# Optimization experiments

Hardware: AMD Instinct MI355X
Metric: run time of the kernel (lower is better)

## Reference

```python
import jax, jax.numpy as jnp
import numpy as np

N_NODES = 50000
N_EDGES = 800000
IN_CH = 128
HIDDEN = 16
HEADS = 8
OUT_CH = 128
EDGE_DIM = 16


def _lin_params(key, fan_in, fan_out, bias=True):
    k1, k2 = jax.random.split(key)
    s = 1.0 / np.sqrt(fan_in)
    W = jax.random.uniform(k1, (fan_in, fan_out), jnp.float32, -s, s)
    if bias:
        b = jax.random.uniform(k2, (fan_out,), jnp.float32, -s, s)
        return W, b
    return W


def setup_inputs() -> dict:
    key = jax.random.key(0)
    ks = jax.random.split(key, 16)
    x = jax.random.normal(ks[0], (N_NODES, IN_CH), jnp.float32)
    edge_index = jax.random.randint(ks[1], (2, N_EDGES), 0, N_NODES, jnp.int64)
    edge_attr = jax.random.normal(ks[2], (N_EDGES, EDGE_DIM), jnp.float32)
    HC0 = HEADS * HIDDEN
    Wq0, bq0 = _lin_params(ks[3], IN_CH, HC0)
    Wk0, bk0 = _lin_params(ks[4], IN_CH, HC0)
    Wv0, bv0 = _lin_params(ks[5], IN_CH, HC0)
    We0 = _lin_params(ks[6], EDGE_DIM, HC0, bias=False)
    Ws0, bs0 = _lin_params(ks[7], IN_CH, HC0)
    Wq1, bq1 = _lin_params(ks[8], HC0, OUT_CH)
    Wk1, bk1 = _lin_params(ks[9], HC0, OUT_CH)
    Wv1, bv1 = _lin_params(ks[10], HC0, OUT_CH)
    We1 = _lin_params(ks[11], EDGE_DIM, OUT_CH, bias=False)
    Ws1, bs1 = _lin_params(ks[12], HC0, OUT_CH)
    return dict(x=x, edge_index=edge_index, edge_attr=edge_attr,
                Wq0=Wq0, bq0=bq0, Wk0=Wk0, bk0=bk0, Wv0=Wv0, bv0=bv0, We0=We0, Ws0=Ws0, bs0=bs0,
                Wq1=Wq1, bq1=bq1, Wk1=Wk1, bk1=bk1, Wv1=Wv1, bv1=bv1, We1=We1, Ws1=Ws1, bs1=bs1)


def transformer_conv(x, src, dst, edge_attr, Wq, bq, Wk, bk, Wv, bv, We, Ws, bs, heads, concat):
    """PyG TransformerConv: gather-attend-softmax(per dst)-scatter, edge features added to key/value."""
    N = x.shape[0]
    E = src.shape[0]
    C = Wq.shape[1] // heads
    q = (x @ Wq + bq).reshape(N, heads, C)
    k = (x @ Wk + bk).reshape(N, heads, C)
    v = (x @ Wv + bv).reshape(N, heads, C)
    e = (edge_attr @ We).reshape(E, heads, C)
    key_e = k[src] + e                                  # [E,H,C]
    alpha = jnp.sum(q[dst] * key_e, axis=-1) / jnp.sqrt(jnp.asarray(C, x.dtype))  # [E,H]
    # segment softmax over incoming edges of each dst node
    m = jax.ops.segment_max(alpha, dst, num_segments=N)       # [N,H]
    p = jnp.exp(alpha - m[dst])
    denom = jax.ops.segment_sum(p, dst, num_segments=N)       # [N,H]
    w = p / (denom[dst] + 1e-16)                              # [E,H]
    msg = (v[src] + e) * w[..., None]                         # [E,H,C]
    agg = jax.ops.segment_sum(msg.reshape(E, heads * C), dst, num_segments=N).reshape(N, heads, C)
    out = agg.reshape(N, heads * C) if concat else agg.mean(axis=1)
    return out + (x @ Ws + bs)                                # root skip connection


def reference(x, edge_index, edge_attr,
              Wq0, bq0, Wk0, bk0, Wv0, bv0, We0, Ws0, bs0,
              Wq1, bq1, Wk1, bk1, Wv1, bv1, We1, Ws1, bs1):
    src, dst = edge_index[0], edge_index[1]
    h = transformer_conv(x, src, dst, edge_attr, Wq0, bq0, Wk0, bk0, Wv0, bv0, We0, Ws0, bs0,
                         heads=HEADS, concat=True)
    h = jax.nn.relu(h)
    out = transformer_conv(h, src, dst, edge_attr, Wq1, bq1, Wk1, bk1, Wv1, bv1, We1, Ws1, bs1,
                           heads=1, concat=False)
    return out
```

## Files before the change

### kernel.cpp

```cpp
#include <hip/hip_runtime.h>
#include <stdint.h>

#define N_NODES 50000
#define N_EDGES 800000

typedef __bf16 bf16x8 __attribute__((ext_vector_type(8)));
typedef float f32x4 __attribute__((ext_vector_type(4)));

__device__ __forceinline__ unsigned short f2bf(float f) {
  union { float f; unsigned int i; } x; x.f = f;
  unsigned int i = x.i;
  unsigned int r = (i + 0x7fffu + ((i >> 16) & 1u)) >> 16;
  return (unsigned short)r;
}
__device__ __forceinline__ float bfl(unsigned int p) {
  union { unsigned int i; float f; } x; x.i = p << 16; return x.f;
}
__device__ __forceinline__ float bfh(unsigned int p) {
  union { unsigned int i; float f; } x; x.i = p & 0xffff0000u; return x.f;
}

struct Ptr8 { const float* p[8]; };

__global__ __launch_bounds__(256) void transpose_w(Ptr8 ws, unsigned short* wt) {
  int mat = blockIdx.x;
  const float* W = ws.p[mat];
  unsigned short* out = wt + mat * 16384;
  for (int it = 0; it < 64; ++it) {
    int idx = it * 256 + threadIdx.x;
    int n = idx >> 7, k = idx & 127;
    out[n * 128 + k] = f2bf(W[k * 128 + n]);
  }
}

__global__ void zero_kernel(int* cnt, int* cursor, int* pad) {
  int i = blockIdx.x * blockDim.x + threadIdx.x;
  if (i < N_NODES) { cnt[i] = 0; cursor[i] = 0; }
  if (i < 16) pad[i] = 0;
}

__global__ void hist_kernel(const int* __restrict__ dst, int* __restrict__ cnt) {
  int e = blockIdx.x * blockDim.x + threadIdx.x;
  if (e < N_EDGES) atomicAdd(&cnt[dst[e]], 1);
}

__global__ __launch_bounds__(1024) void scan_kernel(const int* __restrict__ cnt, int* __restrict__ rs) {
  const int n = N_NODES, per = 49;
  int t = threadIdx.x;
  int lo = t * per; int hi = lo + per;
  if (lo > n) lo = n;
  if (hi > n) hi = n;
  int s = 0;
  for (int i = lo; i < hi; ++i) s += cnt[i];
  int lane = t & 63, wv = t >> 6;
  int v = s;
  #pragma unroll
  for (int off = 1; off < 64; off <<= 1) {
    int u = __shfl_up(v, off, 64);
    if (lane >= off) v += u;
  }
  __shared__ int wsum[16], woff[16];
  if (lane == 63) wsum[wv] = v;
  __syncthreads();
  if (t == 0) { int a = 0; for (int w = 0; w < 16; ++w) { woff[w] = a; a += wsum[w]; } }
  __syncthreads();
  int run = woff[wv] + (v - s);
  if (t == 0) rs[0] = 0;
  for (int i = lo; i < hi; ++i) { run += cnt[i]; rs[i + 1] = run; }
}

__global__ void scatter_kernel(const int* __restrict__ src, const int* __restrict__ dst,
                               const int* __restrict__ rs, int* __restrict__ cursor,
                               int2* __restrict__ eidx2) {
  int e = blockIdx.x * blockDim.x + threadIdx.x;
  if (e < N_EDGES) {
    int d = dst[e];
    int pos = rs[d] + atomicAdd(&cursor[d], 1);
    eidx2[pos] = make_int2(src[e], e);
  }
}

struct GemmArgs {
  const float* Xf;
  const unsigned short* Xh;
  const unsigned short* Wt;
  const float* b0; const float* b1; const float* b2; const float* b3;
  unsigned short* qb;
  unsigned short* kvb;
  unsigned short* sb;
  int M;
};

template<bool XF32>
__global__ __launch_bounds__(256) void node_gemm(GemmArgs ga) {
  __shared__ alignas(16) unsigned short At[128 * 128];
  __shared__ alignas(16) unsigned short Bt[128 * 128];
  int which = blockIdx.y;
  const unsigned short* Wt = ga.Wt + which * 16384;
  int m0 = blockIdx.x * 128;

  #pragma unroll
  for (int it = 0; it < 8; ++it) {
    int c = it * 256 + threadIdx.x;
    int row = c >> 4, slot = c & 15;
    int dsl = slot ^ (row & 7);
    int grow = m0 + row; if (grow >= ga.M) grow = ga.M - 1;
    alignas(16) unsigned short tmp[8];
    if (XF32) {
      const float* xp = ga.Xf + (size_t)grow * 128 + slot * 8;
      float4 a = *(const float4*)xp;
      float4 b = *(const float4*)(xp + 4);
      tmp[0] = f2bf(a.x); tmp[1] = f2bf(a.y); tmp[2] = f2bf(a.z); tmp[3] = f2bf(a.w);
      tmp[4] = f2bf(b.x); tmp[5] = f2bf(b.y); tmp[6] = f2bf(b.z); tmp[7] = f2bf(b.w);
    } else {
      *(uint4*)tmp = *(const uint4*)(ga.Xh + (size_t)grow * 128 + slot * 8);
    }
    *(uint4*)(&At[row * 128 + dsl * 8]) = *(const uint4*)tmp;
    *(uint4*)(&Bt[row * 128 + dsl * 8]) = *(const uint4*)(Wt + c * 8);
  }
  __syncthreads();

  int lane = threadIdx.x & 63, wv = threadIdx.x >> 6;
  int wm = wv >> 1, wn = wv & 1;
  int lr = lane & 15, lk = lane >> 4;
  f32x4 acc[4][4];
  #pragma unroll
  for (int mi = 0; mi < 4; ++mi)
    #pragma unroll
    for (int ni = 0; ni < 4; ++ni) acc[mi][ni] = (f32x4){0.f, 0.f, 0.f, 0.f};

  #pragma unroll
  for (int kk = 0; kk < 4; ++kk) {
    bf16x8 af[4], bfr[4];
    #pragma unroll
    for (int mi = 0; mi < 4; ++mi) {
      int row = wm * 64 + mi * 16 + lr;
      int slot = (kk * 4 + lk) ^ (row & 7);
      af[mi] = *(const bf16x8*)(&At[row * 128 + slot * 8]);
    }
    #pragma unroll
    for (int ni = 0; ni < 4; ++ni) {
      int row = wn * 64 + ni * 16 + lr;
      int slot = (kk * 4 + lk) ^ (row & 7);
      bfr[ni] = *(const bf16x8*)(&Bt[row * 128 + slot * 8]);
    }
    #pragma unroll
    for (int mi = 0; mi < 4; ++mi)
      #pragma unroll
      for (int ni = 0; ni < 4; ++ni)
        acc[mi][ni] = __builtin_amdgcn_mfma_f32_16x16x32_bf16(af[mi], bfr[ni], acc[mi][ni], 0, 0, 0);
  }

  const float* bias = which == 0 ? ga.b0 : which == 1 ? ga.b1 : which == 2 ? ga.b2 : ga.b3;
  float bv[4];
  #pragma unroll
  for (int ni = 0; ni < 4; ++ni) bv[ni] = bias[wn * 64 + ni * 16 + lr];
  #pragma unroll
  for (int mi = 0; mi < 4; ++mi) {
    #pragma unroll
    for (int i = 0; i < 4; ++i) {
      int row = m0 + wm * 64 + mi * 16 + lk * 4 + i;
      if (row < ga.M) {
        #pragma unroll
        for (int ni = 0; ni < 4; ++ni) {
          int col = wn * 64 + ni * 16 + lr;
          unsigned short val = f2bf(acc[mi][ni][i] + bv[ni]);
          if (which == 0)      ga.qb[(size_t)row * 128 + col] = val;
          else if (which == 3) ga.sb[(size_t)row * 128 + col] = val;
          else {
            size_t base = (size_t)row * 256 + (size_t)(col >> 1) * 4 + (col & 1);
            ga.kvb[base + (which == 2 ? 2 : 0)] = val;
          }
        }
      }
    }
  }
}

template<int CHALF, bool RELU, bool OUT_BF16>
__global__ __launch_bounds__(256) void edge_attn(
    const unsigned short* __restrict__ Q, const uint2* __restrict__ KV,
    const unsigned short* __restrict__ S, const float* __restrict__ We,
    const float* __restrict__ EA, const int2* __restrict__ eidx2,
    const int* __restrict__ rs, void* __restrict__ outv, float inv_sqrt_c) {
  int wv = threadIdx.x >> 6, lane = threadIdx.x & 63;
  int node = blockIdx.x * 4 + wv;
  if (node >= N_NODES) return;
  int c0 = lane * 2;
  int jbase = (lane & 1) * 8 + ((lane >> 1) & 1) * 4 + ((lane >> 2) & 1) * 2;

  unsigned int qp = *(const unsigned int*)(Q + (size_t)node * 128 + c0);
  float qa = bfl(qp) * inv_sqrt_c;
  float qb = bfh(qp) * inv_sqrt_c;

  float part[16];
  #pragma unroll
  for (int j = 0; j < 16; ++j) {
    float2 wp = *(const float2*)(We + j * 128 + c0);
    part[j] = qa * wp.x + qb * wp.y;
  }
  {
    bool hi = lane & 1;
    #pragma unroll
    for (int j = 0; j < 8; ++j) {
      float kept = hi ? part[j + 8] : part[j];
      float sent = hi ? part[j] : part[j + 8];
      part[j] = kept + __shfl_xor(sent, 1, 64);
    }
    hi = lane & 2;
    #pragma unroll
    for (int j = 0; j < 4; ++j) {
      float kept = hi ? part[j + 4] : part[j];
      float sent = hi ? part[j] : part[j + 4];
      part[j] = kept + __shfl_xor(sent, 2, 64);
    }
    hi = lane & 4;
    #pragma unroll
    for (int j = 0; j < 2; ++j) {
      float kept = hi ? part[j + 2] : part[j];
      float sent = hi ? part[j] : part[j + 2];
      part[j] = kept + __shfl_xor(sent, 4, 64);
    }
  }
  if (CHALF == 64) {
    #pragma unroll
    for (int s = 8; s <= 32; s <<= 1) {
      part[0] += __shfl_xor(part[0], s, 64);
      part[1] += __shfl_xor(part[1], s, 64);
    }
  }
  float qw0 = part[0] * (CHALF == 64 ? 0.125f : 1.0f);
  float qw1 = part[1] * (CHALF == 64 ? 0.125f : 1.0f);

  int i0 = rs[node], i1 = rs[node + 1];
  int deg = i1 - i0;
  float den = 0.f, a0 = 0.f, a1 = 0.f, wea0 = 0.f, wea1 = 0.f;

  struct Buf { uint2 kv[8]; float ea0[8]; float ea1[8]; };
  Buf bA, bB;
  int2 ceA, ceB;

  auto load_ce = [&](int c) -> int2 {
    return eidx2[i0 + c * 8 + (lane & 7)];
  };
  auto gather = [&](Buf& b, const int2& ce) {
    #pragma unroll
    for (int j = 0; j < 8; ++j) {
      int sv = __shfl(ce.x, j, 64);
      int ei = __shfl(ce.y, j, 64);
      b.kv[j] = KV[(size_t)sv * 64 + lane];
      float2 ep = *(const float2*)(EA + (size_t)ei * 16 + jbase);
      b.ea0[j] = ep.x; b.ea1[j] = ep.y;
    }
  };
  auto compute = [&](const Buf& b, int c) {
    #pragma unroll
    for (int j = 0; j < 8; ++j) {
      int g = i0 + c * 8 + j;
      uint2 kv = b.kv[j];
      float p = qa * bfl(kv.x) + qb * bfh(kv.x) + qw0 * b.ea0[j] + qw1 * b.ea1[j];
      #pragma unroll
      for (int off = 1; off < CHALF; off <<= 1) p += __shfl_xor(p, off, 64);
      float w = (g < i1) ? __expf(p) : 0.f;
      den  += w;
      a0   += w * bfl(kv.y);
      a1   += w * bfh(kv.y);
      wea0 += w * b.ea0[j];
      wea1 += w * b.ea1[j];
    }
  };

  int nch = (deg + 7) >> 3;
  if (nch > 0) {
    ceA = load_ce(0);
    if (nch > 1) ceB = load_ce(1);
    gather(bA, ceA);
    int c = 0;
    while (true) {
      if (c + 1 < nch) gather(bB, ceB);
      if (c + 2 < nch) ceA = load_ce(c + 2);
      compute(bA, c);
      ++c; if (c >= nch) break;
      if (c + 1 < nch) gather(bA, ceA);
      if (c + 2 < nch) ceB = load_ce(c + 2);
      compute(bB, c);
      ++c; if (c >= nch) break;
    }
  }

  float inv = 1.f / (den + 1e-16f);
  float eadd0 = 0.f, eadd1 = 0.f;
  #pragma unroll
  for (int j = 0; j < 16; ++j) {
    int owner = ((j >> 3) & 1) | (((j >> 2) & 1) << 1) | (((j >> 1) & 1) << 2);
    int srcl = (lane & 56) | owner;
    float val = __shfl((j & 1) ? wea1 : wea0, srcl, 64);
    float2 wp = *(const float2*)(We + j * 128 + c0);
    eadd0 += val * wp.x;
    eadd1 += val * wp.y;
  }
  unsigned int sp = *(const unsigned int*)(S + (size_t)node * 128 + c0);
  float o0 = (a0 + eadd0) * inv + bfl(sp);
  float o1 = (a1 + eadd1) * inv + bfh(sp);
  if (RELU) { o0 = fmaxf(o0, 0.f); o1 = fmaxf(o1, 0.f); }
  if (OUT_BF16) {
    unsigned int op = ((unsigned int)f2bf(o1) << 16) | (unsigned int)f2bf(o0);
    *(unsigned int*)((unsigned short*)outv + (size_t)node * 128 + c0) = op;
  } else {
    *(float2*)((float*)outv + (size_t)node * 128 + c0) = make_float2(o0, o1);
  }
}

extern "C" void kernel_launch(void* const* d_in, const int* in_sizes, int n_in,
                              void* d_out, int out_size, void* d_ws, size_t ws_size,
                              hipStream_t stream) {
  const float* x   = (const float*)d_in[0];
  const int*   ei  = (const int*)d_in[1];
  const float* ea  = (const float*)d_in[2];
  const float* Wq0 = (const float*)d_in[3];
  const float* bq0 = (const float*)d_in[4];
  const float* Wk0 = (const float*)d_in[5];
  const float* bk0 = (const float*)d_in[6];
  const float* Wv0 = (const float*)d_in[7];
  const float* bv0 = (const float*)d_in[8];
  const float* We0 = (const float*)d_in[9];
  const float* Ws0 = (const float*)d_in[10];
  const float* bs0 = (const float*)d_in[11];
  const float* Wq1 = (const float*)d_in[12];
  const float* bq1 = (const float*)d_in[13];
  const float* Wk1 = (const float*)d_in[14];
  const float* bk1 = (const float*)d_in[15];
  const float* Wv1 = (const float*)d_in[16];
  const float* bv1 = (const float*)d_in[17];
  const float* We1 = (const float*)d_in[18];
  const float* Ws1 = (const float*)d_in[19];
  const float* bs1 = (const float*)d_in[20];

  char* ws = (char*)d_ws;
  size_t off = 0;
  auto alloc = [&](size_t bytes) -> void* {
    void* p = ws + off;
    off = (off + bytes + 255) & ~(size_t)255;
    return p;
  };
  unsigned short* WT  = (unsigned short*)alloc(8 * 16384 * 2);
  unsigned short* q   = (unsigned short*)alloc((size_t)N_NODES * 128 * 2);
  unsigned short* kvb = (unsigned short*)alloc((size_t)N_NODES * 256 * 2);
  unsigned short* s   = (unsigned short*)alloc((size_t)N_NODES * 128 * 2);
  unsigned short* h   = (unsigned short*)alloc((size_t)N_NODES * 128 * 2);
  int* cnt    = (int*)alloc(N_NODES * 4);
  int* rs     = (int*)alloc((N_NODES + 1) * 4);
  int* cursor = (int*)alloc(N_NODES * 4);
  int2* eidx2 = (int2*)alloc(((size_t)N_EDGES + 8) * 8);

  const int* srcp = ei;
  const int* dstp = ei + N_EDGES;

  Ptr8 p8 = {{Wq0, Wk0, Wv0, Ws0, Wq1, Wk1, Wv1, Ws1}};
  transpose_w<<<8, 256, 0, stream>>>(p8, WT);
  zero_kernel<<<196, 256, 0, stream>>>(cnt, cursor, (int*)(eidx2 + N_EDGES));
  hist_kernel<<<3125, 256, 0, stream>>>(dstp, cnt);
  scan_kernel<<<1, 1024, 0, stream>>>(cnt, rs);
  scatter_kernel<<<3125, 256, 0, stream>>>(srcp, dstp, rs, cursor, eidx2);

  GemmArgs ga0 = { x, nullptr, WT, bq0, bk0, bv0, bs0, q, kvb, s, N_NODES };
  node_gemm<true><<<dim3(391, 4), 256, 0, stream>>>(ga0);
  edge_attn<8, true, true><<<12500, 256, 0, stream>>>(q, (const uint2*)kvb, s, We0,
                                                      ea, eidx2, rs, h, 0.25f);

  GemmArgs ga1 = { nullptr, h, WT + 4 * 16384, bq1, bk1, bv1, bs1, q, kvb, s, N_NODES };
  node_gemm<false><<<dim3(391, 4), 256, 0, stream>>>(ga1);
  edge_attn<64, false, false><<<12500, 256, 0, stream>>>(q, (const uint2*)kvb, s, We1,
                                                         ea, eidx2, rs, d_out, 0.08838834764831845f);
}
```

Baseline: 672.8 us.

## Pre-gather edge attributes into CSR order as bf16 and fuse four node GEMMs

Adds an ea_gather pass that reorders edge_attr into dst-sorted CSR order as bf16. The attention kernels can then read edge features contiguously, without indexing 64-byte fp32 rows through an edge-id indirection. The node GEMM now loads the X tile once and loops over the four weight matrices, instead of launching four grid slices that each reload X. The interleaved KV buffer is split into separate K and V arrays. The cost is an extra pass over edges, about 25.6 MB of extra workspace, and a 4x smaller GEMM grid (391 blocks) that may lower occupancy and parallelism.

```diff
diff --git a/kernel.cpp b/kernel.cpp
--- a/kernel.cpp
+++ b/kernel.cpp
@@ -33,10 +33,11 @@
   }
 }
 
-__global__ void zero_kernel(int* cnt, int* cursor, int* pad) {
+__global__ void zero_kernel(int* cnt, int* cursor, int* srcpad, unsigned int* eapad) {
   int i = blockIdx.x * blockDim.x + threadIdx.x;
   if (i < N_NODES) { cnt[i] = 0; cursor[i] = 0; }
-  if (i < 16) pad[i] = 0;
+  if (i < 8)  srcpad[i] = 0;
+  if (i < 64) eapad[i] = 0;
 }
 
 __global__ void hist_kernel(const int* __restrict__ dst, int* __restrict__ cnt) {
@@ -71,33 +72,45 @@
 
 __global__ void scatter_kernel(const int* __restrict__ src, const int* __restrict__ dst,
                                const int* __restrict__ rs, int* __restrict__ cursor,
-                               int2* __restrict__ eidx2) {
+                               int* __restrict__ srcArr, int* __restrict__ eidxArr) {
   int e = blockIdx.x * blockDim.x + threadIdx.x;
   if (e < N_EDGES) {
     int d = dst[e];
     int pos = rs[d] + atomicAdd(&cursor[d], 1);
-    eidx2[pos] = make_int2(src[e], e);
-  }
-}
-
-struct GemmArgs {
+    srcArr[pos]  = src[e];
+    eidxArr[pos] = e;
+  }
+}
+
+__global__ __launch_bounds__(256) void ea_gather(const float* __restrict__ EA,
+                                                 const int* __restrict__ eidxArr,
+                                                 unsigned short* __restrict__ eacsr) {
+  int r = blockIdx.x * 32 + (threadIdx.x >> 3);
+  if (r >= N_EDGES) return;
+  int j = (threadIdx.x & 7) * 2;
+  int e = eidxArr[r];
+  float2 v = *(const float2*)(EA + (size_t)e * 16 + j);
+  unsigned int pk = (unsigned int)f2bf(v.x) | ((unsigned int)f2bf(v.y) << 16);
+  *(unsigned int*)(eacsr + (size_t)r * 16 + j) = pk;
+}
+
+struct Gemm4Args {
   const float* Xf;
   const unsigned short* Xh;
   const unsigned short* Wt;
-  const float* b0; const float* b1; const float* b2; const float* b3;
-  unsigned short* qb;
-  unsigned short* kvb;
-  unsigned short* sb;
+  const float* b[4];
+  unsigned short* o[4];
   int M;
 };
 
 template<bool XF32>
-__global__ __launch_bounds__(256) void node_gemm(GemmArgs ga) {
+__global__ __launch_bounds__(256) void node_gemm4(Gemm4Args ga) {
   __shared__ alignas(16) unsigned short At[128 * 128];
   __shared__ alignas(16) unsigned short Bt[128 * 128];
-  int which = blockIdx.y;
-  const unsigned short* Wt = ga.Wt + which * 16384;
   int m0 = blockIdx.x * 128;
+  int lane = threadIdx.x & 63, wv = threadIdx.x >> 6;
+  int wm = wv >> 1, wn = wv & 1;
+  int lr = lane & 15, lk = lane >> 4;
 
   #pragma unroll
   for (int it = 0; it < 8; ++it) {
@@ -116,60 +129,64 @@
       *(uint4*)tmp = *(const uint4*)(ga.Xh + (size_t)grow * 128 + slot * 8);
     }
     *(uint4*)(&At[row * 128 + dsl * 8]) = *(const uint4*)tmp;
-    *(uint4*)(&Bt[row * 128 + dsl * 8]) = *(const uint4*)(Wt + c * 8);
-  }
-  __syncthreads();
-
-  int lane = threadIdx.x & 63, wv = threadIdx.x >> 6;
-  int wm = wv >> 1, wn = wv & 1;
-  int lr = lane & 15, lk = lane >> 4;
-  f32x4 acc[4][4];
-  #pragma unroll
-  for (int mi = 0; mi < 4; ++mi)
-    #pragma unroll
-    for (int ni = 0; ni < 4; ++ni) acc[mi][ni] = (f32x4){0.f, 0.f, 0.f, 0.f};
-
-  #pragma unroll
-  for (int kk = 0; kk < 4; ++kk) {
-    bf16x8 af[4], bfr[4];
+  }
+
+  #pragma unroll
+  for (int which = 0; which < 4; ++which) {
+    if (which) __syncthreads();
+    const unsigned short* Wt = ga.Wt + which * 16384;
+    #pragma unroll
+    for (int it = 0; it < 8; ++it) {
+      int c = it * 256 + threadIdx.x;
+      int row = c >> 4, slot = c & 15;
+      int dsl = slot ^ (row & 7);
+      *(uint4*)(&Bt[row * 128 + dsl * 8]) = *(const uint4*)(Wt + c * 8);
+    }
+    __syncthreads();
+
+    f32x4 acc[4][4];
+    #pragma unroll
+    for (int mi = 0; mi < 4; ++mi)
+      #pragma unroll
+      for (int ni = 0; ni < 4; ++ni) acc[mi][ni] = (f32x4){0.f, 0.f, 0.f, 0.f};
+
+    #pragma unroll
+    for (int kk = 0; kk < 4; ++kk) {
+      bf16x8 af[4], bfr[4];
+      #pragma unroll
+      for (int mi = 0; mi < 4; ++mi) {
+        int row = wm * 64 + mi * 16 + lr;
+        int slot = (kk * 4 + lk) ^ (row & 7);
+        af[mi] = *(const bf16x8*)(&At[row * 128 + slot * 8]);
+      }
+      #pragma unroll
+      for (int ni = 0; ni < 4; ++ni) {
+        int row = wn * 64 + ni * 16 + lr;
+        int slot = (kk * 4 + lk) ^ (row & 7);
+        bfr[ni] = *(const bf16x8*)(&Bt[row * 128 + slot * 8]);
+      }
+      #pragma unroll
+      for (int mi = 0; mi < 4; ++mi)
+        #pragma unroll
+        for (int ni = 0; ni < 4; ++ni)
+          acc[mi][ni] = __builtin_amdgcn_mfma_f32_16x16x32_bf16(af[mi], bfr[ni], acc[mi][ni], 0, 0, 0);
+    }
+
+    const float* bias = ga.b[which];
+    unsigned short* outp = ga.o[which];
+    float bv[4];
+    #pragma unroll
+    for (int ni = 0; ni < 4; ++ni) bv[ni] = bias[wn * 64 + ni * 16 + lr];
     #pragma unroll
     for (int mi = 0; mi < 4; ++mi) {
-      int row = wm * 64 + mi * 16 + lr;
-      int slot = (kk * 4 + lk) ^ (row & 7);
-      af[mi] = *(const bf16x8*)(&At[row * 128 + slot * 8]);
-    }
-    #pragma unroll
-    for (int ni = 0; ni < 4; ++ni) {
-      int row = wn * 64 + ni * 16 + lr;
-      int slot = (kk * 4 + lk) ^ (row & 7);
-      bfr[ni] = *(const bf16x8*)(&Bt[row * 128 + slot * 8]);
-    }
-    #pragma unroll
-    for (int mi = 0; mi < 4; ++mi)
-      #pragma unroll
-      for (int ni = 0; ni < 4; ++ni)
-        acc[mi][ni] = __builtin_amdgcn_mfma_f32_16x16x32_bf16(af[mi], bfr[ni], acc[mi][ni], 0, 0, 0);
-  }
-
-  const float* bias = which == 0 ? ga.b0 : which == 1 ? ga.b1 : which == 2 ? ga.b2 : ga.b3;
-  float bv[4];
-  #pragma unroll
-  for (int ni = 0; ni < 4; ++ni) bv[ni] = bias[wn * 64 + ni * 16 + lr];
-  #pragma unroll
-  for (int mi = 0; mi < 4; ++mi) {
-    #pragma unroll
-    for (int i = 0; i < 4; ++i) {
-      int row = m0 + wm * 64 + mi * 16 + lk * 4 + i;
-      if (row < ga.M) {
-        #pragma unroll
-        for (int ni = 0; ni < 4; ++ni) {
-          int col = wn * 64 + ni * 16 + lr;
-          unsigned short val = f2bf(acc[mi][ni][i] + bv[ni]);
-          if (which == 0)      ga.qb[(size_t)row * 128 + col] = val;
-          else if (which == 3) ga.sb[(size_t)row * 128 + col] = val;
-          else {
-            size_t base = (size_t)row * 256 + (size_t)(col >> 1) * 4 + (col & 1);
-            ga.kvb[base + (which == 2 ? 2 : 0)] = val;
+      #pragma unroll
+      for (int i = 0; i < 4; ++i) {
+        int row = m0 + wm * 64 + mi * 16 + lk * 4 + i;
+        if (row < ga.M) {
+          #pragma unroll
+          for (int ni = 0; ni < 4; ++ni) {
+            int col = wn * 64 + ni * 16 + lr;
+            outp[(size_t)row * 128 + col] = f2bf(acc[mi][ni][i] + bv[ni]);
           }
         }
       }
@@ -179,10 +196,11 @@
 
 template<int CHALF, bool RELU, bool OUT_BF16>
 __global__ __launch_bounds__(256) void edge_attn(
-    const unsigned short* __restrict__ Q, const uint2* __restrict__ KV,
-    const unsigned short* __restrict__ S, const float* __restrict__ We,
-    const float* __restrict__ EA, const int2* __restrict__ eidx2,
-    const int* __restrict__ rs, void* __restrict__ outv, float inv_sqrt_c) {
+    const unsigned short* __restrict__ Q, const unsigned short* __restrict__ Kb,
+    const unsigned short* __restrict__ Vb, const unsigned short* __restrict__ S,
+    const float* __restrict__ We, const unsigned short* __restrict__ EAC,
+    const int* __restrict__ srcArr, const int* __restrict__ rs,
+    void* __restrict__ outv, float inv_sqrt_c) {
   int wv = threadIdx.x >> 6, lane = threadIdx.x & 63;
   int node = blockIdx.x * 4 + wv;
   if (node >= N_NODES) return;
@@ -190,6 +208,7 @@
   int jbase = (lane & 1) * 8 + ((lane >> 1) & 1) * 4 + ((lane >> 2) & 1) * 2;
 
   unsigned int qp = *(const unsigned int*)(Q + (size_t)node * 128 + c0);
+  unsigned int sp = *(const unsigned int*)(S + (size_t)node * 128 + c0);
   float qa = bfl(qp) * inv_sqrt_c;
   float qb = bfh(qp) * inv_sqrt_c;
 
@@ -236,53 +255,52 @@
   int deg = i1 - i0;
   float den = 0.f, a0 = 0.f, a1 = 0.f, wea0 = 0.f, wea1 = 0.f;
 
-  struct Buf { uint2 kv[8]; float ea0[8]; float ea1[8]; };
+  struct Buf { unsigned int kp[8], vp[8], ep[8]; };
   Buf bA, bB;
-  int2 ceA, ceB;
-
-  auto load_ce = [&](int c) -> int2 {
-    return eidx2[i0 + c * 8 + (lane & 7)];
+  int svA = 0, svB = 0;
+
+  auto load_src = [&](int c) -> int {
+    return srcArr[i0 + c * 8 + (lane & 7)];
   };
-  auto gather = [&](Buf& b, const int2& ce) {
+  auto gather = [&](Buf& b, int c, int sv) {
     #pragma unroll
     for (int j = 0; j < 8; ++j) {
-      int sv = __shfl(ce.x, j, 64);
-      int ei = __shfl(ce.y, j, 64);
-      b.kv[j] = KV[(size_t)sv * 64 + lane];
-      float2 ep = *(const float2*)(EA + (size_t)ei * 16 + jbase);
-      b.ea0[j] = ep.x; b.ea1[j] = ep.y;
+      int s = __shfl(sv, j, 8);
+      b.kp[j] = *(const unsigned int*)(Kb + (size_t)s * 128 + c0);
+      b.vp[j] = *(const unsigned int*)(Vb + (size_t)s * 128 + c0);
+      b.ep[j] = *(const unsigned int*)(EAC + (size_t)(i0 + c * 8 + j) * 16 + jbase);
     }
   };
   auto compute = [&](const Buf& b, int c) {
     #pragma unroll
     for (int j = 0; j < 8; ++j) {
       int g = i0 + c * 8 + j;
-      uint2 kv = b.kv[j];
-      float p = qa * bfl(kv.x) + qb * bfh(kv.x) + qw0 * b.ea0[j] + qw1 * b.ea1[j];
+      float ea0 = bfl(b.ep[j]), ea1 = bfh(b.ep[j]);
+      float p = qa * bfl(b.kp[j]) + qb * bfh(b.kp[j]) + qw0 * ea0 + qw1 * ea1;
       #pragma unroll
       for (int off = 1; off < CHALF; off <<= 1) p += __shfl_xor(p, off, 64);
       float w = (g < i1) ? __expf(p) : 0.f;
       den  += w;
-      a0   += w * bfl(kv.y);
-      a1   += w * bfh(kv.y);
-      wea0 += w * b.ea0[j];
-      wea1 += w * b.ea1[j];
+      a0   += w * bfl(b.vp[j]);
+      a1   += w * bfh(b.vp[j]);
+      wea0 += w * ea0;
+      wea1 += w * ea1;
     }
   };
 
   int nch = (deg + 7) >> 3;
   if (nch > 0) {
-    ceA = load_ce(0);
-    if (nch > 1) ceB = load_ce(1);
-    gather(bA, ceA);
+    svA = load_src(0);
+    if (nch > 1) svB = load_src(1);
+    gather(bA, 0, svA);
     int c = 0;
     while (true) {
-      if (c + 1 < nch) gather(bB, ceB);
-      if (c + 2 < nch) ceA = load_ce(c + 2);
+      if (c + 1 < nch) gather(bB, c + 1, svB);
+      if (c + 2 < nch) svA = load_src(c + 2);
       compute(bA, c);
       ++c; if (c >= nch) break;
-      if (c + 1 < nch) gather(bA, ceA);
-      if (c + 2 < nch) ceB = load_ce(c + 2);
+      if (c + 1 < nch) gather(bA, c + 1, svA);
+      if (c + 2 < nch) svB = load_src(c + 2);
       compute(bB, c);
       ++c; if (c >= nch) break;
     }
@@ -299,7 +317,6 @@
     eadd0 += val * wp.x;
     eadd1 += val * wp.y;
   }
-  unsigned int sp = *(const unsigned int*)(S + (size_t)node * 128 + c0);
   float o0 = (a0 + eadd0) * inv + bfl(sp);
   float o1 = (a1 + eadd1) * inv + bfh(sp);
   if (RELU) { o0 = fmaxf(o0, 0.f); o1 = fmaxf(o1, 0.f); }
@@ -343,33 +360,38 @@
     off = (off + bytes + 255) & ~(size_t)255;
     return p;
   };
-  unsigned short* WT  = (unsigned short*)alloc(8 * 16384 * 2);
-  unsigned short* q   = (unsigned short*)alloc((size_t)N_NODES * 128 * 2);
-  unsigned short* kvb = (unsigned short*)alloc((size_t)N_NODES * 256 * 2);
-  unsigned short* s   = (unsigned short*)alloc((size_t)N_NODES * 128 * 2);
-  unsigned short* h   = (unsigned short*)alloc((size_t)N_NODES * 128 * 2);
-  int* cnt    = (int*)alloc(N_NODES * 4);
-  int* rs     = (int*)alloc((N_NODES + 1) * 4);
-  int* cursor = (int*)alloc(N_NODES * 4);
-  int2* eidx2 = (int2*)alloc(((size_t)N_EDGES + 8) * 8);
+  unsigned short* WT    = (unsigned short*)alloc(8 * 16384 * 2);
+  unsigned short* q     = (unsigned short*)alloc((size_t)N_NODES * 128 * 2);
+  unsigned short* k     = (unsigned short*)alloc((size_t)N_NODES * 128 * 2);
+  unsigned short* v     = (unsigned short*)alloc((size_t)N_NODES * 128 * 2);
+  unsigned short* s     = (unsigned short*)alloc((size_t)N_NODES * 128 * 2);
+  unsigned short* h     = (unsigned short*)alloc((size_t)N_NODES * 128 * 2);
+  unsigned short* eacsr = (unsigned short*)alloc(((size_t)N_EDGES + 8) * 16 * 2);
+  int* cnt     = (int*)alloc(N_NODES * 4);
+  int* rs      = (int*)alloc((N_NODES + 1) * 4);
+  int* cursor  = (int*)alloc(N_NODES * 4);
+  int* srcArr  = (int*)alloc(((size_t)N_EDGES + 8) * 4);
+  int* eidxArr = (int*)alloc((size_t)N_EDGES * 4);
 
   const int* srcp = ei;
   const int* dstp = ei + N_EDGES;
 
   Ptr8 p8 = {{Wq0, Wk0, Wv0, Ws0, Wq1, Wk1, Wv1, Ws1}};
   transpose_w<<<8, 256, 0, stream>>>(p8, WT);
-  zero_kernel<<<196, 256, 0, stream>>>(cnt, cursor, (int*)(eidx2 + N_EDGES));
+  zero_kernel<<<196, 256, 0, stream>>>(cnt, cursor, srcArr + N_EDGES,
+                                       (unsigned int*)(eacsr + (size_t)N_EDGES * 16));
   hist_kernel<<<3125, 256, 0, stream>>>(dstp, cnt);
   scan_kernel<<<1, 1024, 0, stream>>>(cnt, rs);
-  scatter_kernel<<<3125, 256, 0, stream>>>(srcp, dstp, rs, cursor, eidx2);
-
-  GemmArgs ga0 = { x, nullptr, WT, bq0, bk0, bv0, bs0, q, kvb, s, N_NODES };
-  node_gemm<true><<<dim3(391, 4), 256, 0, stream>>>(ga0);
-  edge_attn<8, true, true><<<12500, 256, 0, stream>>>(q, (const uint2*)kvb, s, We0,
-                                                      ea, eidx2, rs, h, 0.25f);
-
-  GemmArgs ga1 = { nullptr, h, WT + 4 * 16384, bq1, bk1, bv1, bs1, q, kvb, s, N_NODES };
-  node_gemm<false><<<dim3(391, 4), 256, 0, stream>>>(ga1);
-  edge_attn<64, false, false><<<12500, 256, 0, stream>>>(q, (const uint2*)kvb, s, We1,
-                                                         ea, eidx2, rs, d_out, 0.08838834764831845f);
-}
+  scatter_kernel<<<3125, 256, 0, stream>>>(srcp, dstp, rs, cursor, srcArr, eidxArr);
+  ea_gather<<<25000, 256, 0, stream>>>(ea, eidxArr, eacsr);
+
+  Gemm4Args ga0 = { x, nullptr, WT, {bq0, bk0, bv0, bs0}, {q, k, v, s}, N_NODES };
+  node_gemm4<true><<<391, 256, 0, stream>>>(ga0);
+  edge_attn<8, true, true><<<12500, 256, 0, stream>>>(q, k, v, s, We0, eacsr,
+                                                      srcArr, rs, h, 0.25f);
+
+  Gemm4Args ga1 = { nullptr, h, WT + 4 * 16384, {bq1, bk1, bv1, bs1}, {q, k, v, s}, N_NODES };
+  node_gemm4<false><<<391, 256, 0, stream>>>(ga1);
+  edge_attn<64, false, false><<<12500, 256, 0, stream>>>(q, k, v, s, We1, eacsr,
+                                                         srcArr, rs, d_out, 0.08838834764831845f);
+}
```

Result: faster. 639.0 us (-5.0%).
